# Performance work log

Measured on AMD Instinct MI355X. Metric: run time of the kernel, lower is better.

The kernel has to match this reference:

```python
import jax, jax.numpy as jnp
import numpy as np

E, H, D = 64, 128, 2  # embedding_dim, hidden_dim, input_dim
PRED_LEN = 60


def lstm_cell(x, h, c, W_ih, W_hh, b_ih, b_hh):
    # PyTorch gate order: i, f, g, o
    gates = x @ W_ih.T + h @ W_hh.T + b_ih + b_hh  # (B, 4H)
    i, f, g, o = jnp.split(gates, 4, axis=-1)
    i = jax.nn.sigmoid(i)
    f = jax.nn.sigmoid(f)
    g = jnp.tanh(g)
    o = jax.nn.sigmoid(o)
    c = f * c + i * g
    h = o * jnp.tanh(c)
    return h, c


def setup_inputs() -> dict:
    key = jax.random.key(0)
    ks = jax.random.split(key, 12)
    B, T = 4096, 50
    s = lambda *sh: 1.0 / np.sqrt(sh[-1])
    inp = {
        "history": jax.random.normal(ks[0], (B, T, D), jnp.float32),
        "W_emb": jax.random.normal(ks[1], (E, D), jnp.float32) * s(E, D),
        "b_emb": jnp.zeros((E,), jnp.float32),
        "W_ih": jax.random.normal(ks[2], (4 * H, E), jnp.float32) * s(4 * H, E),
        "W_hh": jax.random.normal(ks[3], (4 * H, H), jnp.float32) * s(4 * H, H),
        "b_ih": jnp.zeros((4 * H,), jnp.float32),
        "b_hh": jnp.zeros((4 * H,), jnp.float32),
        "W1": jax.random.normal(ks[4], (H, H), jnp.float32) * s(H, H),
        "b1": jnp.zeros((H,), jnp.float32),
        "W2": jax.random.normal(ks[5], (D, H), jnp.float32) * s(D, H),
        "b2": jnp.zeros((D,), jnp.float32),
    }
    return inp


def reference(history, W_emb, b_emb, W_ih, W_hh, b_ih, b_hh, W1, b1, W2, b2):
    B = history.shape[0]
    # Input embedding for the whole history at once: (B, T, E)
    hist_embed = history @ W_emb.T + b_emb

    # --- Encoder LSTM over history ---
    h0 = jnp.zeros((B, H), history.dtype)
    c0 = jnp.zeros((B, H), history.dtype)

    def enc_step(carry, x_t):
        h, c = carry
        h, c = lstm_cell(x_t, h, c, W_ih, W_hh, b_ih, b_hh)
        return (h, c), None

    (h, c), _ = jax.lax.scan(enc_step, (h0, c0), jnp.swapaxes(hist_embed, 0, 1))

    prev = jnp.zeros((B, E), history.dtype)  # initial zero embedding

    def dec_step(carry, _):
        h, c, prev = carry
        h, c = lstm_cell(prev, h, c, W_ih, W_hh, b_ih, b_hh)
        hid = jax.nn.relu(h @ W1.T + b1)
        pred = hid @ W2.T + b2  # (B, D)
        prev = pred @ W_emb.T + b_emb
        return (h, c, prev), pred

    _, preds = jax.lax.scan(dec_step, (h, c, prev), None, length=PRED_LEN)
    return jnp.swapaxes(preds, 0, 1)  # (B, PRED_LEN, D)
```

## Files before the change

kernel.cpp:

```cpp
#include <hip/hip_runtime.h>
#include <math.h>

#define T_ENC 50
#define T_DEC 60
#define HID   128
#define EMB   64
#define DIN   2
#define MT    16
#define NTHR  512
#define HS    136

typedef __attribute__((ext_vector_type(8))) short frag8;
typedef __attribute__((ext_vector_type(4))) float f32x4;

__device__ __forceinline__ float fast_rcp(float x) { return __builtin_amdgcn_rcpf(x); }
__device__ __forceinline__ float sigm(float x) { return fast_rcp(1.f + __expf(-x)); }
__device__ __forceinline__ float tanh_fast(float x) { return fmaf(2.f, fast_rcp(1.f + __expf(-2.f * x)), -1.f); }

__device__ __forceinline__ void load_wfrag(const float* __restrict__ wrow,
                                           frag8& Fhi, frag8& Flo) {
    union { unsigned short s[8]; frag8 f; } hi, lo;
#pragma unroll
    for (int j = 0; j < 8; ++j) {
        float x      = wrow[j];
        unsigned u   = __float_as_uint(x);
        unsigned uhi = u & 0xffff0000u;
        float    lof = x - __uint_as_float(uhi);
        hi.s[j] = (unsigned short)(uhi >> 16);
        lo.s[j] = (unsigned short)(__float_as_uint(lof) >> 16);
    }
    Fhi = hi.f; Flo = lo.f;
}

__device__ __forceinline__ void split2(float x, unsigned short& hi, unsigned short& lo) {
    unsigned u   = __float_as_uint(x);
    unsigned uhi = u & 0xffff0000u;
    float    lof = x - __uint_as_float(uhi);
    hi = (unsigned short)(uhi >> 16);
    lo = (unsigned short)(__float_as_uint(lof) >> 16);
}

__global__ __launch_bounds__(NTHR, 2) void lstm_all(
    const float* __restrict__ history,
    const float* __restrict__ W_emb,
    const float* __restrict__ b_emb,
    const float* __restrict__ W_ih,
    const float* __restrict__ W_hh,
    const float* __restrict__ b_ih,
    const float* __restrict__ b_hh,
    const float* __restrict__ W1,
    const float* __restrict__ b1,
    const float* __restrict__ w2,
    const float* __restrict__ b2,
    float* __restrict__ out)
{
    __shared__ __align__(16) unsigned short hhi[2][MT * HS];
    __shared__ __align__(16) unsigned short hlo[2][MT * HS];
    __shared__ float hist_s[MT * T_ENC * DIN];
    __shared__ float pred_buf[MT * T_DEC * DIN];
    __shared__ float2 part_s[8][MT];
    __shared__ float wemb_s[EMB * DIN];
    __shared__ float bemb_s[EMB];

    const int tid = threadIdx.x;
    const int L   = tid & 63;
    const int w   = tid >> 6;
    const int nc  = L & 15;
    const int kb0 = (L >> 4) * 8;
    const int m0c = (L >> 4) * 4;
    const int r0  = blockIdx.x * MT;
    const int jcol = w * 16 + nc;

    for (int i = tid; i < MT * T_ENC * DIN; i += NTHR)
        hist_s[i] = history[r0 * T_ENC * DIN + i];
    for (int i = tid; i < MT * HS; i += NTHR) {
        hhi[0][i] = 0; hlo[0][i] = 0;
        hhi[1][i] = 0; hlo[1][i] = 0;
    }
    if (tid < EMB * DIN) wemb_s[tid] = W_emb[tid];
    if (tid < EMB) bemb_s[tid] = b_emb[tid];

    frag8 Bg[4][4][2];
#pragma unroll
    for (int g = 0; g < 4; ++g)
#pragma unroll
        for (int ks = 0; ks < 4; ++ks) {
            int n = g * HID + jcol;
            load_wfrag(&W_hh[(size_t)n * HID + ks * 32 + kb0], Bg[g][ks][0], Bg[g][ks][1]);
        }
    frag8 Bw1[4][2];
#pragma unroll
    for (int ks = 0; ks < 4; ++ks)
        load_wfrag(&W1[(size_t)jcol * HID + ks * 32 + kb0], Bw1[ks][0], Bw1[ks][1]);

    __syncthreads();

    float we0v[4], we1v[4], bs0v[4], bs1v[4];
#pragma unroll
    for (int g = 0; g < 4; ++g) {
        int n = g * HID + jcol;
        float s0 = 0.f, s1 = 0.f, sb = 0.f;
        const float* wr = &W_ih[(size_t)n * EMB];
#pragma unroll 4
        for (int e4 = 0; e4 < EMB / 4; ++e4) {
            float4 wv = *(const float4*)&wr[e4 * 4];
            int e = e4 * 4;
            s0 += wv.x * wemb_s[(e+0)*2] + wv.y * wemb_s[(e+1)*2]
                + wv.z * wemb_s[(e+2)*2] + wv.w * wemb_s[(e+3)*2];
            s1 += wv.x * wemb_s[(e+0)*2+1] + wv.y * wemb_s[(e+1)*2+1]
                + wv.z * wemb_s[(e+2)*2+1] + wv.w * wemb_s[(e+3)*2+1];
            sb += wv.x * bemb_s[e+0] + wv.y * bemb_s[e+1]
                + wv.z * bemb_s[e+2] + wv.w * bemb_s[e+3];
        }
        float b = b_ih[n] + b_hh[n];
        bs0v[g] = b;
        bs1v[g] = b + sb;
        we0v[g] = s0; we1v[g] = s1;
    }
    const float b1v  = b1[jcol];
    const float w2v0 = w2[jcol];
    const float w2v1 = w2[HID + jcol];
    const float b2v0 = b2[0], b2v1 = b2[1];
    const int   fb   = nc * HS + kb0;
    float cst[4] = {0.f, 0.f, 0.f, 0.f};
    int pb = 0;

#pragma unroll 1
    for (int t = 0; t < T_ENC; ++t) {
        f32x4 acc[4];
        float q0[4], q1[4];
#pragma unroll
        for (int r = 0; r < 4; ++r) {
            float2 q = *(const float2*)&hist_s[(m0c + r) * (T_ENC * DIN) + t * DIN];
            q0[r] = q.x; q1[r] = q.y;
        }
#pragma unroll
        for (int g = 0; g < 4; ++g)
#pragma unroll
            for (int r = 0; r < 4; ++r)
                acc[g][r] = fmaf(q1[r], we1v[g], fmaf(q0[r], we0v[g], bs1v[g]));

        const unsigned short* Hh = hhi[pb];
        const unsigned short* Hl = hlo[pb];
#pragma unroll
        for (int ks = 0; ks < 4; ++ks) {
            frag8 Ahi = *(const frag8*)(Hh + fb + ks * 32);
            frag8 Alo = *(const frag8*)(Hl + fb + ks * 32);
#pragma unroll
            for (int g = 0; g < 4; ++g)
                acc[g] = __builtin_amdgcn_mfma_f32_16x16x32_bf16(Ahi, Bg[g][ks][1], acc[g], 0, 0, 0);
#pragma unroll
            for (int g = 0; g < 4; ++g)
                acc[g] = __builtin_amdgcn_mfma_f32_16x16x32_bf16(Alo, Bg[g][ks][0], acc[g], 0, 0, 0);
#pragma unroll
            for (int g = 0; g < 4; ++g)
                acc[g] = __builtin_amdgcn_mfma_f32_16x16x32_bf16(Ahi, Bg[g][ks][0], acc[g], 0, 0, 0);
        }

        const int nb = pb ^ 1;
#pragma unroll
        for (int r = 0; r < 4; ++r) {
            float i_ = sigm(acc[0][r]);
            float f_ = sigm(acc[1][r]);
            float gv = tanh_fast(acc[2][r]);
            float o_ = sigm(acc[3][r]);
            cst[r] = fmaf(f_, cst[r], i_ * gv);
            float h = o_ * tanh_fast(cst[r]);
            unsigned short phi, plo;
            split2(h, phi, plo);
            hhi[nb][(m0c + r) * HS + jcol] = phi;
            hlo[nb][(m0c + r) * HS + jcol] = plo;
        }
        pb = nb;
        __syncthreads();
    }

#pragma unroll 1
    for (int it = 0; it < T_DEC; ++it) {
        f32x4 acc[4];
        f32x4 hacc = (f32x4){b1v, b1v, b1v, b1v};
#pragma unroll
        for (int g = 0; g < 4; ++g) {
            float b = (it == 0) ? bs0v[g] : bs1v[g];
            acc[g] = (f32x4){b, b, b, b};
        }

        const unsigned short* Hh = hhi[pb];
        const unsigned short* Hl = hlo[pb];
        if (it == 0) {
#pragma unroll
            for (int ks = 0; ks < 4; ++ks) {
                frag8 Ahi = *(const frag8*)(Hh + fb + ks * 32);
                frag8 Alo = *(const frag8*)(Hl + fb + ks * 32);
#pragma unroll
                for (int g = 0; g < 4; ++g)
                    acc[g] = __builtin_amdgcn_mfma_f32_16x16x32_bf16(Ahi, Bg[g][ks][1], acc[g], 0, 0, 0);
#pragma unroll
                for (int g = 0; g < 4; ++g)
                    acc[g] = __builtin_amdgcn_mfma_f32_16x16x32_bf16(Alo, Bg[g][ks][0], acc[g], 0, 0, 0);
#pragma unroll
                for (int g = 0; g < 4; ++g)
                    acc[g] = __builtin_amdgcn_mfma_f32_16x16x32_bf16(Ahi, Bg[g][ks][0], acc[g], 0, 0, 0);
            }
        } else {
#pragma unroll
            for (int ks = 0; ks < 4; ++ks) {
                frag8 Ahi = *(const frag8*)(Hh + fb + ks * 32);
                frag8 Alo = *(const frag8*)(Hl + fb + ks * 32);
#pragma unroll
                for (int g = 0; g < 4; ++g)
                    acc[g] = __builtin_amdgcn_mfma_f32_16x16x32_bf16(Ahi, Bg[g][ks][1], acc[g], 0, 0, 0);
                hacc = __builtin_amdgcn_mfma_f32_16x16x32_bf16(Ahi, Bw1[ks][1], hacc, 0, 0, 0);
#pragma unroll
                for (int g = 0; g < 4; ++g)
                    acc[g] = __builtin_amdgcn_mfma_f32_16x16x32_bf16(Alo, Bg[g][ks][0], acc[g], 0, 0, 0);
                hacc = __builtin_amdgcn_mfma_f32_16x16x32_bf16(Alo, Bw1[ks][0], hacc, 0, 0, 0);
#pragma unroll
                for (int g = 0; g < 4; ++g)
                    acc[g] = __builtin_amdgcn_mfma_f32_16x16x32_bf16(Ahi, Bg[g][ks][0], acc[g], 0, 0, 0);
                hacc = __builtin_amdgcn_mfma_f32_16x16x32_bf16(Ahi, Bw1[ks][0], hacc, 0, 0, 0);
            }

            float p0[4], p1[4];
#pragma unroll
            for (int r = 0; r < 4; ++r) {
                float hv = fmaxf(hacc[r], 0.f);
                p0[r] = hv * w2v0;
                p1[r] = hv * w2v1;
            }
#pragma unroll
            for (int mask = 1; mask < 16; mask <<= 1)
#pragma unroll
                for (int r = 0; r < 4; ++r) {
                    p0[r] += __shfl_xor(p0[r], mask);
                    p1[r] += __shfl_xor(p1[r], mask);
                }
            if (nc == 0)
#pragma unroll
                for (int r = 0; r < 4; ++r)
                    part_s[w][m0c + r] = (float2){p0[r], p1[r]};
            __syncthreads();

            if (tid < 32) {
                int m = tid >> 1, d = tid & 1;
                float s = (d == 0) ? b2v0 : b2v1;
#pragma unroll
                for (int wi = 0; wi < 8; ++wi) {
                    float2 v = part_s[wi][m];
                    s += (d == 0) ? v.x : v.y;
                }
                pred_buf[(m * T_DEC + (it - 1)) * DIN + d] = s;
            }
            __syncthreads();

#pragma unroll
            for (int r = 0; r < 4; ++r) {
                float2 pq = *(const float2*)&pred_buf[((m0c + r) * T_DEC + (it - 1)) * DIN];
#pragma unroll
                for (int g = 0; g < 4; ++g)
                    acc[g][r] += fmaf(pq.y, we1v[g], pq.x * we0v[g]);
            }
        }

        const int nb = pb ^ 1;
#pragma unroll
        for (int r = 0; r < 4; ++r) {
            float i_ = sigm(acc[0][r]);
            float f_ = sigm(acc[1][r]);
            float gv = tanh_fast(acc[2][r]);
            float o_ = sigm(acc[3][r]);
            cst[r] = fmaf(f_, cst[r], i_ * gv);
            float h = o_ * tanh_fast(cst[r]);
            unsigned short phi, plo;
            split2(h, phi, plo);
            hhi[nb][(m0c + r) * HS + jcol] = phi;
            hlo[nb][(m0c + r) * HS + jcol] = plo;
        }
        pb = nb;
        __syncthreads();
    }

    {
        f32x4 hacc = (f32x4){b1v, b1v, b1v, b1v};
        const unsigned short* Hh = hhi[pb];
        const unsigned short* Hl = hlo[pb];
#pragma unroll
        for (int ks = 0; ks < 4; ++ks) {
            frag8 Ahi = *(const frag8*)(Hh + fb + ks * 32);
            frag8 Alo = *(const frag8*)(Hl + fb + ks * 32);
            hacc = __builtin_amdgcn_mfma_f32_16x16x32_bf16(Ahi, Bw1[ks][1], hacc, 0, 0, 0);
            hacc = __builtin_amdgcn_mfma_f32_16x16x32_bf16(Alo, Bw1[ks][0], hacc, 0, 0, 0);
            hacc = __builtin_amdgcn_mfma_f32_16x16x32_bf16(Ahi, Bw1[ks][0], hacc, 0, 0, 0);
        }
        float p0[4], p1[4];
#pragma unroll
        for (int r = 0; r < 4; ++r) {
            float hv = fmaxf(hacc[r], 0.f);
            p0[r] = hv * w2v0;
            p1[r] = hv * w2v1;
        }
#pragma unroll
        for (int mask = 1; mask < 16; mask <<= 1)
#pragma unroll
            for (int r = 0; r < 4; ++r) {
                p0[r] += __shfl_xor(p0[r], mask);
                p1[r] += __shfl_xor(p1[r], mask);
            }
        if (nc == 0)
#pragma unroll
            for (int r = 0; r < 4; ++r)
                part_s[w][m0c + r] = (float2){p0[r], p1[r]};
        __syncthreads();
        if (tid < 32) {
            int m = tid >> 1, d = tid & 1;
            float s = (d == 0) ? b2v0 : b2v1;
#pragma unroll
            for (int wi = 0; wi < 8; ++wi) {
                float2 v = part_s[wi][m];
                s += (d == 0) ? v.x : v.y;
            }
            pred_buf[(m * T_DEC + (T_DEC - 1)) * DIN + d] = s;
        }
        __syncthreads();
    }

    for (int i = tid; i < MT * T_DEC * DIN; i += NTHR)
        out[(size_t)r0 * T_DEC * DIN + i] = pred_buf[i];
}

extern "C" void kernel_launch(void* const* d_in, const int* in_sizes, int n_in,
                              void* d_out, int out_size, void* d_ws, size_t ws_size,
                              hipStream_t stream) {
    const float* history = (const float*)d_in[0];
    const float* W_emb   = (const float*)d_in[1];
    const float* b_emb   = (const float*)d_in[2];
    const float* W_ih    = (const float*)d_in[3];
    const float* W_hh    = (const float*)d_in[4];
    const float* b_ih    = (const float*)d_in[5];
    const float* b_hh    = (const float*)d_in[6];
    const float* W1      = (const float*)d_in[7];
    const float* b1      = (const float*)d_in[8];
    const float* W2      = (const float*)d_in[9];
    const float* b2      = (const float*)d_in[10];
    float* out = (float*)d_out;
    (void)d_ws; (void)ws_size; (void)in_sizes; (void)n_in; (void)out_size;

    lstm_all<<<4096 / MT, NTHR, 0, stream>>>(history, W_emb, b_emb, W_ih, W_hh,
                                             b_ih, b_hh, W1, b1, W2, b2, out);
}
```

Before: 353.0 us.

## Remove per-step decoder barrier by redundant per-thread prediction reduction

Every thread now reduces the per-wave partial predictions from shared memory itself, using vector loads. Before, 32 threads did this reduction and an extra block barrier followed. This removes one __syncthreads per decoder step. The change also peels decoder step 0 out of the loop, switches to pointer-swapped double buffers, issues the first A-fragment loads early in each step, and puts sched barriers into the weight preload. The cost is redundant LDS reads and adds across all threads.

After: 390.0 us. 1.1x slower.

```diff
diff --git a/kernel.cpp b/kernel.cpp
--- a/kernel.cpp
+++ b/kernel.cpp
@@ -58,7 +58,7 @@
     __shared__ __align__(16) unsigned short hlo[2][MT * HS];
     __shared__ float hist_s[MT * T_ENC * DIN];
     __shared__ float pred_buf[MT * T_DEC * DIN];
-    __shared__ float2 part_s[8][MT];
+    __shared__ __align__(16) float2 part_s[8][MT];
     __shared__ float wemb_s[EMB * DIN];
     __shared__ float bemb_s[EMB];
 
@@ -82,16 +82,19 @@
 
     frag8 Bg[4][4][2];
 #pragma unroll
-    for (int g = 0; g < 4; ++g)
+    for (int g = 0; g < 4; ++g) {
 #pragma unroll
         for (int ks = 0; ks < 4; ++ks) {
             int n = g * HID + jcol;
             load_wfrag(&W_hh[(size_t)n * HID + ks * 32 + kb0], Bg[g][ks][0], Bg[g][ks][1]);
         }
+        __builtin_amdgcn_sched_barrier(0);
+    }
     frag8 Bw1[4][2];
 #pragma unroll
     for (int ks = 0; ks < 4; ++ks)
         load_wfrag(&W1[(size_t)jcol * HID + ks * 32 + kb0], Bw1[ks][0], Bw1[ks][1]);
+    __builtin_amdgcn_sched_barrier(0);
 
     __syncthreads();
 
@@ -123,10 +126,17 @@
     const float b2v0 = b2[0], b2v1 = b2[1];
     const int   fb   = nc * HS + kb0;
     float cst[4] = {0.f, 0.f, 0.f, 0.f};
-    int pb = 0;
+
+    const unsigned short* Hh = hhi[0];
+    const unsigned short* Hl = hlo[0];
+    unsigned short* Nh = hhi[1];
+    unsigned short* Nl = hlo[1];
 
 #pragma unroll 1
     for (int t = 0; t < T_ENC; ++t) {
+        frag8 Ahi0 = *(const frag8*)(Hh + fb);
+        frag8 Alo0 = *(const frag8*)(Hl + fb);
+
         f32x4 acc[4];
         float q0[4], q1[4];
 #pragma unroll
@@ -140,12 +150,10 @@
             for (int r = 0; r < 4; ++r)
                 acc[g][r] = fmaf(q1[r], we1v[g], fmaf(q0[r], we0v[g], bs1v[g]));
 
-        const unsigned short* Hh = hhi[pb];
-        const unsigned short* Hl = hlo[pb];
-#pragma unroll
-        for (int ks = 0; ks < 4; ++ks) {
-            frag8 Ahi = *(const frag8*)(Hh + fb + ks * 32);
-            frag8 Alo = *(const frag8*)(Hl + fb + ks * 32);
+#pragma unroll
+        for (int ks = 0; ks < 4; ++ks) {
+            frag8 Ahi = (ks == 0) ? Ahi0 : *(const frag8*)(Hh + fb + ks * 32);
+            frag8 Alo = (ks == 0) ? Alo0 : *(const frag8*)(Hl + fb + ks * 32);
 #pragma unroll
             for (int g = 0; g < 4; ++g)
                 acc[g] = __builtin_amdgcn_mfma_f32_16x16x32_bf16(Ahi, Bg[g][ks][1], acc[g], 0, 0, 0);
@@ -157,7 +165,6 @@
                 acc[g] = __builtin_amdgcn_mfma_f32_16x16x32_bf16(Ahi, Bg[g][ks][0], acc[g], 0, 0, 0);
         }
 
-        const int nb = pb ^ 1;
 #pragma unroll
         for (int r = 0; r < 4; ++r) {
             float i_ = sigm(acc[0][r]);
@@ -168,101 +175,33 @@
             float h = o_ * tanh_fast(cst[r]);
             unsigned short phi, plo;
             split2(h, phi, plo);
-            hhi[nb][(m0c + r) * HS + jcol] = phi;
-            hlo[nb][(m0c + r) * HS + jcol] = plo;
-        }
-        pb = nb;
-        __syncthreads();
-    }
-
-#pragma unroll 1
-    for (int it = 0; it < T_DEC; ++it) {
+            Nh[(m0c + r) * HS + jcol] = phi;
+            Nl[(m0c + r) * HS + jcol] = plo;
+        }
+        { const unsigned short* th = Hh; Hh = Nh; Nh = (unsigned short*)th;
+          const unsigned short* tl = Hl; Hl = Nl; Nl = (unsigned short*)tl; }
+        __syncthreads();
+    }
+
+    {
         f32x4 acc[4];
-        f32x4 hacc = (f32x4){b1v, b1v, b1v, b1v};
-#pragma unroll
-        for (int g = 0; g < 4; ++g) {
-            float b = (it == 0) ? bs0v[g] : bs1v[g];
-            acc[g] = (f32x4){b, b, b, b};
-        }
-
-        const unsigned short* Hh = hhi[pb];
-        const unsigned short* Hl = hlo[pb];
-        if (it == 0) {
-#pragma unroll
-            for (int ks = 0; ks < 4; ++ks) {
-                frag8 Ahi = *(const frag8*)(Hh + fb + ks * 32);
-                frag8 Alo = *(const frag8*)(Hl + fb + ks * 32);
-#pragma unroll
-                for (int g = 0; g < 4; ++g)
-                    acc[g] = __builtin_amdgcn_mfma_f32_16x16x32_bf16(Ahi, Bg[g][ks][1], acc[g], 0, 0, 0);
-#pragma unroll
-                for (int g = 0; g < 4; ++g)
-                    acc[g] = __builtin_amdgcn_mfma_f32_16x16x32_bf16(Alo, Bg[g][ks][0], acc[g], 0, 0, 0);
-#pragma unroll
-                for (int g = 0; g < 4; ++g)
-                    acc[g] = __builtin_amdgcn_mfma_f32_16x16x32_bf16(Ahi, Bg[g][ks][0], acc[g], 0, 0, 0);
-            }
-        } else {
-#pragma unroll
-            for (int ks = 0; ks < 4; ++ks) {
-                frag8 Ahi = *(const frag8*)(Hh + fb + ks * 32);
-                frag8 Alo = *(const frag8*)(Hl + fb + ks * 32);
-#pragma unroll
-                for (int g = 0; g < 4; ++g)
-                    acc[g] = __builtin_amdgcn_mfma_f32_16x16x32_bf16(Ahi, Bg[g][ks][1], acc[g], 0, 0, 0);
-                hacc = __builtin_amdgcn_mfma_f32_16x16x32_bf16(Ahi, Bw1[ks][1], hacc, 0, 0, 0);
-#pragma unroll
-                for (int g = 0; g < 4; ++g)
-                    acc[g] = __builtin_amdgcn_mfma_f32_16x16x32_bf16(Alo, Bg[g][ks][0], acc[g], 0, 0, 0);
-                hacc = __builtin_amdgcn_mfma_f32_16x16x32_bf16(Alo, Bw1[ks][0], hacc, 0, 0, 0);
-#pragma unroll
-                for (int g = 0; g < 4; ++g)
-                    acc[g] = __builtin_amdgcn_mfma_f32_16x16x32_bf16(Ahi, Bg[g][ks][0], acc[g], 0, 0, 0);
-                hacc = __builtin_amdgcn_mfma_f32_16x16x32_bf16(Ahi, Bw1[ks][0], hacc, 0, 0, 0);
-            }
-
-            float p0[4], p1[4];
-#pragma unroll
-            for (int r = 0; r < 4; ++r) {
-                float hv = fmaxf(hacc[r], 0.f);
-                p0[r] = hv * w2v0;
-                p1[r] = hv * w2v1;
-            }
-#pragma unroll
-            for (int mask = 1; mask < 16; mask <<= 1)
-#pragma unroll
-                for (int r = 0; r < 4; ++r) {
-                    p0[r] += __shfl_xor(p0[r], mask);
-                    p1[r] += __shfl_xor(p1[r], mask);
-                }
-            if (nc == 0)
-#pragma unroll
-                for (int r = 0; r < 4; ++r)
-                    part_s[w][m0c + r] = (float2){p0[r], p1[r]};
-            __syncthreads();
-
-            if (tid < 32) {
-                int m = tid >> 1, d = tid & 1;
-                float s = (d == 0) ? b2v0 : b2v1;
-#pragma unroll
-                for (int wi = 0; wi < 8; ++wi) {
-                    float2 v = part_s[wi][m];
-                    s += (d == 0) ? v.x : v.y;
-                }
-                pred_buf[(m * T_DEC + (it - 1)) * DIN + d] = s;
-            }
-            __syncthreads();
-
-#pragma unroll
-            for (int r = 0; r < 4; ++r) {
-                float2 pq = *(const float2*)&pred_buf[((m0c + r) * T_DEC + (it - 1)) * DIN];
-#pragma unroll
-                for (int g = 0; g < 4; ++g)
-                    acc[g][r] += fmaf(pq.y, we1v[g], pq.x * we0v[g]);
-            }
-        }
-
-        const int nb = pb ^ 1;
+#pragma unroll
+        for (int g = 0; g < 4; ++g)
+            acc[g] = (f32x4){bs0v[g], bs0v[g], bs0v[g], bs0v[g]};
+#pragma unroll
+        for (int ks = 0; ks < 4; ++ks) {
+            frag8 Ahi = *(const frag8*)(Hh + fb + ks * 32);
+            frag8 Alo = *(const frag8*)(Hl + fb + ks * 32);
+#pragma unroll
+            for (int g = 0; g < 4; ++g)
+                acc[g] = __builtin_amdgcn_mfma_f32_16x16x32_bf16(Ahi, Bg[g][ks][1], acc[g], 0, 0, 0);
+#pragma unroll
+            for (int g = 0; g < 4; ++g)
+                acc[g] = __builtin_amdgcn_mfma_f32_16x16x32_bf16(Alo, Bg[g][ks][0], acc[g], 0, 0, 0);
+#pragma unroll
+            for (int g = 0; g < 4; ++g)
+                acc[g] = __builtin_amdgcn_mfma_f32_16x16x32_bf16(Ahi, Bg[g][ks][0], acc[g], 0, 0, 0);
+        }
 #pragma unroll
         for (int r = 0; r < 4; ++r) {
             float i_ = sigm(acc[0][r]);
@@ -273,17 +212,106 @@
             float h = o_ * tanh_fast(cst[r]);
             unsigned short phi, plo;
             split2(h, phi, plo);
-            hhi[nb][(m0c + r) * HS + jcol] = phi;
-            hlo[nb][(m0c + r) * HS + jcol] = plo;
-        }
-        pb = nb;
+            Nh[(m0c + r) * HS + jcol] = phi;
+            Nl[(m0c + r) * HS + jcol] = plo;
+        }
+        { const unsigned short* th = Hh; Hh = Nh; Nh = (unsigned short*)th;
+          const unsigned short* tl = Hl; Hl = Nl; Nl = (unsigned short*)tl; }
+        __syncthreads();
+    }
+
+#pragma unroll 1
+    for (int it = 1; it < T_DEC; ++it) {
+        frag8 Ahi0 = *(const frag8*)(Hh + fb);
+        frag8 Alo0 = *(const frag8*)(Hl + fb);
+
+        f32x4 acc[4];
+        f32x4 hacc = (f32x4){b1v, b1v, b1v, b1v};
+#pragma unroll
+        for (int g = 0; g < 4; ++g)
+            acc[g] = (f32x4){bs1v[g], bs1v[g], bs1v[g], bs1v[g]};
+
+#pragma unroll
+        for (int ks = 0; ks < 4; ++ks) {
+            frag8 Ahi = (ks == 0) ? Ahi0 : *(const frag8*)(Hh + fb + ks * 32);
+            frag8 Alo = (ks == 0) ? Alo0 : *(const frag8*)(Hl + fb + ks * 32);
+#pragma unroll
+            for (int g = 0; g < 4; ++g)
+                acc[g] = __builtin_amdgcn_mfma_f32_16x16x32_bf16(Ahi, Bg[g][ks][1], acc[g], 0, 0, 0);
+            hacc = __builtin_amdgcn_mfma_f32_16x16x32_bf16(Ahi, Bw1[ks][1], hacc, 0, 0, 0);
+#pragma unroll
+            for (int g = 0; g < 4; ++g)
+                acc[g] = __builtin_amdgcn_mfma_f32_16x16x32_bf16(Alo, Bg[g][ks][0], acc[g], 0, 0, 0);
+            hacc = __builtin_amdgcn_mfma_f32_16x16x32_bf16(Alo, Bw1[ks][0], hacc, 0, 0, 0);
+#pragma unroll
+            for (int g = 0; g < 4; ++g)
+                acc[g] = __builtin_amdgcn_mfma_f32_16x16x32_bf16(Ahi, Bg[g][ks][0], acc[g], 0, 0, 0);
+            hacc = __builtin_amdgcn_mfma_f32_16x16x32_bf16(Ahi, Bw1[ks][0], hacc, 0, 0, 0);
+        }
+
+        float p0[4], p1[4];
+#pragma unroll
+        for (int r = 0; r < 4; ++r) {
+            float hv = fmaxf(hacc[r], 0.f);
+            p0[r] = hv * w2v0;
+            p1[r] = hv * w2v1;
+        }
+#pragma unroll
+        for (int mask = 1; mask < 16; mask <<= 1)
+#pragma unroll
+            for (int r = 0; r < 4; ++r) {
+                p0[r] += __shfl_xor(p0[r], mask);
+                p1[r] += __shfl_xor(p1[r], mask);
+            }
+        if (nc == 0)
+#pragma unroll
+            for (int r = 0; r < 4; ++r)
+                part_s[w][m0c + r] = (float2){p0[r], p1[r]};
+        __syncthreads();
+
+        float pr0[4] = {b2v0, b2v0, b2v0, b2v0};
+        float pr1[4] = {b2v1, b2v1, b2v1, b2v1};
+#pragma unroll
+        for (int wi = 0; wi < 8; ++wi) {
+            f32x4 va = *(const f32x4*)&part_s[wi][m0c];
+            f32x4 vb = *(const f32x4*)&part_s[wi][m0c + 2];
+            pr0[0] += va.x; pr1[0] += va.y;
+            pr0[1] += va.z; pr1[1] += va.w;
+            pr0[2] += vb.x; pr1[2] += vb.y;
+            pr0[3] += vb.z; pr1[3] += vb.w;
+        }
+        if (w == 0 && nc == 0)
+#pragma unroll
+            for (int r = 0; r < 4; ++r)
+                *(float2*)&pred_buf[((m0c + r) * T_DEC + (it - 1)) * DIN] =
+                    (float2){pr0[r], pr1[r]};
+
+#pragma unroll
+        for (int g = 0; g < 4; ++g)
+#pragma unroll
+            for (int r = 0; r < 4; ++r)
+                acc[g][r] += fmaf(pr1[r], we1v[g], pr0[r] * we0v[g]);
+
+#pragma unroll
+        for (int r = 0; r < 4; ++r) {
+            float i_ = sigm(acc[0][r]);
+            float f_ = sigm(acc[1][r]);
+            float gv = tanh_fast(acc[2][r]);
+            float o_ = sigm(acc[3][r]);
+            cst[r] = fmaf(f_, cst[r], i_ * gv);
+            float h = o_ * tanh_fast(cst[r]);
+            unsigned short phi, plo;
+            split2(h, phi, plo);
+            Nh[(m0c + r) * HS + jcol] = phi;
+            Nl[(m0c + r) * HS + jcol] = plo;
+        }
+        { const unsigned short* th = Hh; Hh = Nh; Nh = (unsigned short*)th;
+          const unsigned short* tl = Hl; Hl = Nl; Nl = (unsigned short*)tl; }
         __syncthreads();
     }
 
     {
         f32x4 hacc = (f32x4){b1v, b1v, b1v, b1v};
-        const unsigned short* Hh = hhi[pb];
-        const unsigned short* Hl = hlo[pb];
 #pragma unroll
         for (int ks = 0; ks < 4; ++ks) {
             frag8 Ahi = *(const frag8*)(Hh + fb + ks * 32);
@@ -311,15 +339,22 @@
             for (int r = 0; r < 4; ++r)
                 part_s[w][m0c + r] = (float2){p0[r], p1[r]};
         __syncthreads();
-        if (tid < 32) {
-            int m = tid >> 1, d = tid & 1;
-            float s = (d == 0) ? b2v0 : b2v1;
+        if (w == 0 && nc == 0) {
+            float pr0[4] = {b2v0, b2v0, b2v0, b2v0};
+            float pr1[4] = {b2v1, b2v1, b2v1, b2v1};
 #pragma unroll
             for (int wi = 0; wi < 8; ++wi) {
-                float2 v = part_s[wi][m];
-                s += (d == 0) ? v.x : v.y;
+                f32x4 va = *(const f32x4*)&part_s[wi][m0c];
+                f32x4 vb = *(const f32x4*)&part_s[wi][m0c + 2];
+                pr0[0] += va.x; pr1[0] += va.y;
+                pr0[1] += va.z; pr1[1] += va.w;
+                pr0[2] += vb.x; pr1[2] += vb.y;
+                pr0[3] += vb.z; pr1[3] += vb.w;
             }
-            pred_buf[(m * T_DEC + (T_DEC - 1)) * DIN + d] = s;
+#pragma unroll
+            for (int r = 0; r < 4; ++r)
+                *(float2*)&pred_buf[((m0c + r) * T_DEC + (T_DEC - 1)) * DIN] =
+                    (float2){pr0[r], pr1[r]};
         }
         __syncthreads();
     }
```
